# Optimization experiments

Measured on AMD Instinct MI355X. Metric: run time of the kernel, lower is better.

Reference implementation:

```python
import jax, jax.numpy as jnp
import numpy as np

B = 1024          # global batch
D = 512           # embedding_size
C = 100000        # num_classes (sum over 8 shards)
S = 64.0          # ArcFace scale
M = 0.5           # ArcFace additive angular margin
EPS = 1e-30


def setup_inputs() -> dict:
    key = jax.random.key(0)
    k1, k2, k3 = jax.random.split(key, 3)
    embeddings = jax.random.normal(k1, (B, D), dtype=jnp.float32)
    weight = jax.random.normal(k2, (C, D), dtype=jnp.float32)
    labels = jax.random.randint(k3, (B,), 0, C, dtype=jnp.int64)
    return {"embeddings": embeddings, "weight": weight, "labels": labels}


def reference(embeddings, weight, labels):
    # normalize(embeddings), normalize(weight) -> cosine logits
    ne = embeddings * jax.lax.rsqrt(jnp.sum(embeddings * embeddings, axis=1, keepdims=True))
    nw = weight * jax.lax.rsqrt(jnp.sum(weight * weight, axis=1, keepdims=True))
    logits = jnp.clip(jnp.einsum("bd,cd->bc", ne, nw), -1.0, 1.0)  # [B, C]

    rows = jnp.arange(B)
    target_logit = logits[rows, labels]
    # ArcFace: cos(theta + m), theta+m clipped to pi (insightface CombinedMarginLoss m2)
    theta = jnp.arccos(jnp.clip(target_logit, -1.0, 1.0))
    new_target = jnp.cos(jnp.minimum(theta + M, jnp.float32(np.pi)))
    logits = logits.at[rows, labels].set(new_target) * S

    # FusedDistCrossEntropy (single-device equivalent): stable softmax,
    # gather target prob, loss = -mean(log(clamp(p_target, 1e-30)))
    logp = jax.nn.log_softmax(logits, axis=1)
    p_target = jnp.exp(logp[rows, labels])
    loss = -jnp.mean(jnp.log(jnp.maximum(p_target, EPS)))
    return loss
```

## Files before the change

kernel.cpp:

```cpp
#include <hip/hip_runtime.h>
#include <hip/hip_bf16.h>
#include <math.h>
#include <stdint.h>

#define B_BATCH   1024
#define D_DIM     512
#define C_CLASSES 100000
#define BM        128
#define BN        128
#define BK        32
#define KITERS    (D_DIM / BK)
#define MTILES    (B_BATCH / BM)
#define NTILES    ((C_CLASSES + BN - 1) / BN)
#define NGROUPS   98
#define GRID_G    (8 * 8 * NGROUPS)
#define WBLK      (C_CLASSES / 8)
#define ABLK      (B_BATCH / 8)
#define LOG2E     1.44269504088896340736f
#define COSM      0.87758256189037276f
#define SINM      0.47942553860420301f
#define NEG_LOG_EPS 69.07755278982137f

typedef short bf16x8 __attribute__((ext_vector_type(8)));
typedef float f32x4  __attribute__((ext_vector_type(4)));

static __device__ __forceinline__ unsigned short f2bf(float f) {
    unsigned int u = __builtin_bit_cast(unsigned int, f);
    u += 0x7fffu + ((u >> 16) & 1u);
    return (unsigned short)(u >> 16);
}

static __device__ __forceinline__ unsigned int pk_rne(float lo, float hi) {
    return (unsigned int)f2bf(lo) | ((unsigned int)f2bf(hi) << 16);
}

static __device__ __forceinline__ unsigned int pk_bf16_trunc(float lo, float hi) {
    return __builtin_amdgcn_perm(__builtin_bit_cast(unsigned int, hi),
                                 __builtin_bit_cast(unsigned int, lo),
                                 0x07060302u);
}

static __device__ __forceinline__ void gld16(const unsigned short* g, unsigned short* l) {
    __builtin_amdgcn_global_load_lds(
        (const __attribute__((address_space(1))) unsigned int*)g,
        (__attribute__((address_space(3))) unsigned int*)l, 16, 0, 0);
}

__global__ __launch_bounds__(256) void prep(const float* __restrict__ W,
                                            const float* __restrict__ E,
                                            unsigned short* __restrict__ Wbf,
                                            unsigned short* __restrict__ Abf,
                                            float* __restrict__ out) {
    const int blk  = blockIdx.x;
    const int wave = threadIdx.x >> 6;
    const int lane = threadIdx.x & 63;
    const bool isW = blk < WBLK;
    if (!isW && blk == WBLK && threadIdx.x == 0) *out = 0.f;

    const float* src = isW ? W : E;
    unsigned short* dst = isW ? Wbf : Abf;
    const int r0 = (isW ? blk : blk - WBLK) * 8 + wave * 2;
    const int r1 = r0 + 1;

    const float4* s0 = (const float4*)(src + (size_t)r0 * D_DIM);
    const float4* s1 = (const float4*)(src + (size_t)r1 * D_DIM);
    float4 a0 = s0[2 * lane], a1 = s0[2 * lane + 1];
    float4 b0 = s1[2 * lane], b1 = s1[2 * lane + 1];

    float sa = a0.x*a0.x + a0.y*a0.y + a0.z*a0.z + a0.w*a0.w
             + a1.x*a1.x + a1.y*a1.y + a1.z*a1.z + a1.w*a1.w;
    float sb = b0.x*b0.x + b0.y*b0.y + b0.z*b0.z + b0.w*b0.w
             + b1.x*b1.x + b1.y*b1.y + b1.z*b1.z + b1.w*b1.w;
    #pragma unroll
    for (int off = 1; off < 64; off <<= 1) {
        sa += __shfl_xor(sa, off);
        sb += __shfl_xor(sb, off);
    }
    float ia = rsqrtf(sa), ib = rsqrtf(sb);
    a0.x *= ia; a0.y *= ia; a0.z *= ia; a0.w *= ia;
    a1.x *= ia; a1.y *= ia; a1.z *= ia; a1.w *= ia;
    b0.x *= ib; b0.y *= ib; b0.z *= ib; b0.w *= ib;
    b1.x *= ib; b1.y *= ib; b1.z *= ib; b1.w *= ib;

    uint4 oa, ob;
    if (isW) {
        oa = (uint4){pk_bf16_trunc(a0.x, a0.y), pk_bf16_trunc(a0.z, a0.w),
                     pk_bf16_trunc(a1.x, a1.y), pk_bf16_trunc(a1.z, a1.w)};
        ob = (uint4){pk_bf16_trunc(b0.x, b0.y), pk_bf16_trunc(b0.z, b0.w),
                     pk_bf16_trunc(b1.x, b1.y), pk_bf16_trunc(b1.z, b1.w)};
    } else {
        oa = (uint4){pk_rne(a0.x, a0.y), pk_rne(a0.z, a0.w),
                     pk_rne(a1.x, a1.y), pk_rne(a1.z, a1.w)};
        ob = (uint4){pk_rne(b0.x, b0.y), pk_rne(b0.z, b0.w),
                     pk_rne(b1.x, b1.y), pk_rne(b1.z, b1.w)};
    }
    ((uint4*)(dst + (size_t)r0 * D_DIM))[lane] = oa;
    ((uint4*)(dst + (size_t)r1 * D_DIM))[lane] = ob;
}

static __device__ __forceinline__ float epi_term(float accv, int col, int lab,
                                                 float* __restrict__ st, int srow) {
    float c = fminf(1.f, fmaxf(-1.f, accv));
    if (col >= C_CLASSES) return 0.f;
    float s = c * 64.0f;
    if (col == lab) {
        float sn = sqrtf(fmaxf(0.f, 1.f - c * c));
        float nm = c * COSM - sn * SINM;
        if (c < -COSM) nm = -1.f;
        s = nm * 64.0f;
        st[srow] = s;
    }
    return exp2f((s - 64.0f) * LOG2E);
}

__global__ __launch_bounds__(256, 4) void gemm_cos(const unsigned short* __restrict__ Abf,
                                                   const unsigned short* __restrict__ Wbf,
                                                   const int* __restrict__ labels,
                                                   float* __restrict__ st,
                                                   float* __restrict__ partial) {
    __shared__ unsigned short As[BM * BK];
    __shared__ unsigned short Bs[BN * BK];
    __shared__ float rowSum[BM];
    __shared__ int   labs[BM];

    const int id = blockIdx.x;
    const int x  = id & 7;
    const int s  = id >> 3;
    const int mt = s & 7;
    const int y  = x + 8 * (s >> 3);
    if (y >= NTILES) return;
    const int m0 = mt * BM;
    const int n0 = y * BN;

    const int tid = threadIdx.x;
    if (tid < BM) { labs[tid] = labels[m0 + tid]; rowSum[tid] = 0.f; }

    const int lane = tid & 63;
    const int wave = tid >> 6;
    const int wm = wave & 1, wn = wave >> 1;
    const int l15 = lane & 15, quad = lane >> 4;

    const int rsub = lane >> 2;
    const int cg   = (lane & 3) * 8;
    const int c0 = wave * 2, c1 = wave * 2 + 1;
    const unsigned short* gA0 = Abf + (size_t)(m0 + c0 * 16 + rsub) * D_DIM + cg;
    const unsigned short* gA1 = Abf + (size_t)(m0 + c1 * 16 + rsub) * D_DIM + cg;
    const int bR0 = min(n0 + c0 * 16 + rsub, C_CLASSES - 1);
    const int bR1 = min(n0 + c1 * 16 + rsub, C_CLASSES - 1);
    const unsigned short* gB0 = Wbf + (size_t)bR0 * D_DIM + cg;
    const unsigned short* gB1 = Wbf + (size_t)bR1 * D_DIM + cg;
    unsigned short* lA0 = &As[c0 * 512];
    unsigned short* lA1 = &As[c1 * 512];
    unsigned short* lB0 = &Bs[c0 * 512];
    unsigned short* lB1 = &Bs[c1 * 512];

    const f32x4 z = (f32x4){0.f, 0.f, 0.f, 0.f};
    f32x4 a00 = z, a01 = z, a02 = z, a03 = z;
    f32x4 a10 = z, a11 = z, a12 = z, a13 = z;
    f32x4 a20 = z, a21 = z, a22 = z, a23 = z;
    f32x4 a30 = z, a31 = z, a32 = z, a33 = z;

    const int aro = (wm * 64 + l15) * BK + quad * 8;
    const int bro = (wn * 64 + l15) * BK + quad * 8;

    for (int kk = 0; kk < KITERS; ++kk) {
        __syncthreads();
        gld16(gA0, lA0); gld16(gA1, lA1);
        gld16(gB0, lB0); gld16(gB1, lB1);
        gA0 += BK; gA1 += BK; gB0 += BK; gB1 += BK;
        __syncthreads();

        bf16x8 af0 = *(const bf16x8*)&As[aro];
        bf16x8 af1 = *(const bf16x8*)&As[aro + 16 * BK];
        bf16x8 af2 = *(const bf16x8*)&As[aro + 32 * BK];
        bf16x8 af3 = *(const bf16x8*)&As[aro + 48 * BK];
        bf16x8 bf0 = *(const bf16x8*)&Bs[bro];
        bf16x8 bf1 = *(const bf16x8*)&Bs[bro + 16 * BK];
        bf16x8 bf2 = *(const bf16x8*)&Bs[bro + 32 * BK];
        bf16x8 bf3 = *(const bf16x8*)&Bs[bro + 48 * BK];

        a00 = __builtin_amdgcn_mfma_f32_16x16x32_bf16(af0, bf0, a00, 0, 0, 0);
        a01 = __builtin_amdgcn_mfma_f32_16x16x32_bf16(af0, bf1, a01, 0, 0, 0);
        a02 = __builtin_amdgcn_mfma_f32_16x16x32_bf16(af0, bf2, a02, 0, 0, 0);
        a03 = __builtin_amdgcn_mfma_f32_16x16x32_bf16(af0, bf3, a03, 0, 0, 0);
        a10 = __builtin_amdgcn_mfma_f32_16x16x32_bf16(af1, bf0, a10, 0, 0, 0);
        a11 = __builtin_amdgcn_mfma_f32_16x16x32_bf16(af1, bf1, a11, 0, 0, 0);
        a12 = __builtin_amdgcn_mfma_f32_16x16x32_bf16(af1, bf2, a12, 0, 0, 0);
        a13 = __builtin_amdgcn_mfma_f32_16x16x32_bf16(af1, bf3, a13, 0, 0, 0);
        a20 = __builtin_amdgcn_mfma_f32_16x16x32_bf16(af2, bf0, a20, 0, 0, 0);
        a21 = __builtin_amdgcn_mfma_f32_16x16x32_bf16(af2, bf1, a21, 0, 0, 0);
        a22 = __builtin_amdgcn_mfma_f32_16x16x32_bf16(af2, bf2, a22, 0, 0, 0);
        a23 = __builtin_amdgcn_mfma_f32_16x16x32_bf16(af2, bf3, a23, 0, 0, 0);
        a30 = __builtin_amdgcn_mfma_f32_16x16x32_bf16(af3, bf0, a30, 0, 0, 0);
        a31 = __builtin_amdgcn_mfma_f32_16x16x32_bf16(af3, bf1, a31, 0, 0, 0);
        a32 = __builtin_amdgcn_mfma_f32_16x16x32_bf16(af3, bf2, a32, 0, 0, 0);
        a33 = __builtin_amdgcn_mfma_f32_16x16x32_bf16(af3, bf3, a33, 0, 0, 0);
    }

    const int colbase = n0 + wn * 64 + l15;

    #define EPIROW(A0, A1, A2, A3, MI)                                         \
    {                                                                          \
        _Pragma("unroll")                                                      \
        for (int r = 0; r < 4; ++r) {                                          \
            const int rloc = wm * 64 + (MI) * 16 + quad * 4 + r;               \
            const int lab = labs[rloc];                                        \
            float part = 0.f;                                                  \
            part += epi_term((A0)[r], colbase,      lab, st, m0 + rloc);       \
            part += epi_term((A1)[r], colbase + 16, lab, st, m0 + rloc);       \
            part += epi_term((A2)[r], colbase + 32, lab, st, m0 + rloc);       \
            part += epi_term((A3)[r], colbase + 48, lab, st, m0 + rloc);       \
            part += __shfl_xor(part, 1);                                       \
            part += __shfl_xor(part, 2);                                       \
            part += __shfl_xor(part, 4);                                       \
            part += __shfl_xor(part, 8);                                       \
            if (l15 == 0) atomicAdd(&rowSum[rloc], part);                      \
        }                                                                      \
    }

    EPIROW(a00, a01, a02, a03, 0)
    EPIROW(a10, a11, a12, a13, 1)
    EPIROW(a20, a21, a22, a23, 2)
    EPIROW(a30, a31, a32, a33, 3)
    #undef EPIROW

    __syncthreads();
    if (tid < BM) partial[(size_t)(m0 + tid) * NTILES + y] = rowSum[tid];
}

__global__ __launch_bounds__(64) void reduce_loss(const float* __restrict__ partial,
                                                  const float* __restrict__ st,
                                                  float* __restrict__ out) {
    const int b = blockIdx.x;
    const int l = threadIdx.x;
    const float* row = partial + (size_t)b * NTILES;
    float L = 0.f;
    for (int t = l; t < NTILES; t += 64) L += row[t];
    #pragma unroll
    for (int off = 1; off < 64; off <<= 1) L += __shfl_xor(L, off);
    if (l == 0) {
        float logp = st[b] - 64.0f - logf(L);
        float lossb = fminf(-logp, NEG_LOG_EPS) * (1.0f / (float)B_BATCH);
        atomicAdd(out, lossb);
    }
}

extern "C" void kernel_launch(void* const* d_in, const int* in_sizes, int n_in,
                              void* d_out, int out_size, void* d_ws, size_t ws_size,
                              hipStream_t stream) {
    const float* emb = (const float*)d_in[0];
    const float* wgt = (const float*)d_in[1];
    const int*   lab = (const int*)d_in[2];
    float* out = (float*)d_out;
    char* ws = (char*)d_ws;

    const size_t WBF_B = (size_t)C_CLASSES * D_DIM * 2;
    const size_t ABF_B = (size_t)B_BATCH * D_DIM * 2;

    unsigned short* Wbf = (unsigned short*)ws;
    unsigned short* Abf = (unsigned short*)(ws + WBF_B);
    float* st      = (float*)(ws + WBF_B + ABF_B);
    float* partial = (float*)(ws + WBF_B + ABF_B + 4096);

    prep<<<WBLK + ABLK, 256, 0, stream>>>(wgt, emb, Wbf, Abf, out);
    gemm_cos<<<GRID_G, 256, 0, stream>>>(Abf, Wbf, lab, st, partial);
    reduce_loss<<<B_BATCH, 64, 0, stream>>>(partial, st, out);
}
```

Before: 452.4 us.

## Double GEMM K-tile to 64 and add XOR-swizzled LDS layout

Raises the per-iteration K slice from 32 to 64, which halves the number of barrier pairs in the main loop and gives two MFMA groups per synchronisation. The global-to-LDS staging is rebuilt with an XOR swizzle on 16-byte column chunks so that the 128-byte LDS rows can be read by the MFMA fragments without bank conflicts. LDS footprint per block doubles, which may reduce occupancy, and the loop is still single-buffered, so loads are not overlapped with compute.

```diff
diff --git a/kernel.cpp b/kernel.cpp
--- a/kernel.cpp
+++ b/kernel.cpp
@@ -8,7 +8,7 @@
 #define C_CLASSES 100000
 #define BM        128
 #define BN        128
-#define BK        32
+#define BK        64
 #define KITERS    (D_DIM / BK)
 #define MTILES    (B_BATCH / BM)
 #define NTILES    ((C_CLASSES + BN - 1) / BN)
@@ -140,19 +140,22 @@
     const int wm = wave & 1, wn = wave >> 1;
     const int l15 = lane & 15, quad = lane >> 4;
 
-    const int rsub = lane >> 2;
-    const int cg   = (lane & 3) * 8;
-    const int c0 = wave * 2, c1 = wave * 2 + 1;
-    const unsigned short* gA0 = Abf + (size_t)(m0 + c0 * 16 + rsub) * D_DIM + cg;
-    const unsigned short* gA1 = Abf + (size_t)(m0 + c1 * 16 + rsub) * D_DIM + cg;
-    const int bR0 = min(n0 + c0 * 16 + rsub, C_CLASSES - 1);
-    const int bR1 = min(n0 + c1 * 16 + rsub, C_CLASSES - 1);
-    const unsigned short* gB0 = Wbf + (size_t)bR0 * D_DIM + cg;
-    const unsigned short* gB1 = Wbf + (size_t)bR1 * D_DIM + cg;
-    unsigned short* lA0 = &As[c0 * 512];
-    unsigned short* lA1 = &As[c1 * 512];
-    unsigned short* lB0 = &Bs[c0 * 512];
-    unsigned short* lB1 = &Bs[c1 * 512];
+    const int rIn = lane >> 3;
+    const int csl = (((lane & 7) ^ rIn) << 4);
+    const char* gA[4];
+    const char* gB[4];
+    unsigned short* lA[4];
+    unsigned short* lB[4];
+    #pragma unroll
+    for (int c = 0; c < 4; ++c) {
+        const int chunk = wave * 4 + c;
+        const int row = chunk * 8 + rIn;
+        gA[c] = (const char*)Abf + (size_t)(m0 + row) * (D_DIM * 2) + csl;
+        const int bRow = min(n0 + row, C_CLASSES - 1);
+        gB[c] = (const char*)Wbf + (size_t)bRow * (D_DIM * 2) + csl;
+        lA[c] = &As[chunk * 512];
+        lB[c] = &Bs[chunk * 512];
+    }
 
     const f32x4 z = (f32x4){0.f, 0.f, 0.f, 0.f};
     f32x4 a00 = z, a01 = z, a02 = z, a03 = z;
@@ -160,41 +163,48 @@
     f32x4 a20 = z, a21 = z, a22 = z, a23 = z;
     f32x4 a30 = z, a31 = z, a32 = z, a33 = z;
 
-    const int aro = (wm * 64 + l15) * BK + quad * 8;
-    const int bro = (wn * 64 + l15) * BK + quad * 8;
+    const char* baseA = (const char*)As + (size_t)(wm * 64 + l15) * 128;
+    const char* baseB = (const char*)Bs + (size_t)(wn * 64 + l15) * 128;
+    const int q0 = ((quad ^ (l15 & 7)) << 4);
 
     for (int kk = 0; kk < KITERS; ++kk) {
         __syncthreads();
-        gld16(gA0, lA0); gld16(gA1, lA1);
-        gld16(gB0, lB0); gld16(gB1, lB1);
-        gA0 += BK; gA1 += BK; gB0 += BK; gB1 += BK;
+        #pragma unroll
+        for (int c = 0; c < 4; ++c) {
+            gld16((const unsigned short*)gA[c], lA[c]); gA[c] += 2 * BK;
+            gld16((const unsigned short*)gB[c], lB[c]); gB[c] += 2 * BK;
+        }
         __syncthreads();
 
-        bf16x8 af0 = *(const bf16x8*)&As[aro];
-        bf16x8 af1 = *(const bf16x8*)&As[aro + 16 * BK];
-        bf16x8 af2 = *(const bf16x8*)&As[aro + 32 * BK];
-        bf16x8 af3 = *(const bf16x8*)&As[aro + 48 * BK];
-        bf16x8 bf0 = *(const bf16x8*)&Bs[bro];
-        bf16x8 bf1 = *(const bf16x8*)&Bs[bro + 16 * BK];
-        bf16x8 bf2 = *(const bf16x8*)&Bs[bro + 32 * BK];
-        bf16x8 bf3 = *(const bf16x8*)&Bs[bro + 48 * BK];
-
-        a00 = __builtin_amdgcn_mfma_f32_16x16x32_bf16(af0, bf0, a00, 0, 0, 0);
-        a01 = __builtin_amdgcn_mfma_f32_16x16x32_bf16(af0, bf1, a01, 0, 0, 0);
-        a02 = __builtin_amdgcn_mfma_f32_16x16x32_bf16(af0, bf2, a02, 0, 0, 0);
-        a03 = __builtin_amdgcn_mfma_f32_16x16x32_bf16(af0, bf3, a03, 0, 0, 0);
-        a10 = __builtin_amdgcn_mfma_f32_16x16x32_bf16(af1, bf0, a10, 0, 0, 0);
-        a11 = __builtin_amdgcn_mfma_f32_16x16x32_bf16(af1, bf1, a11, 0, 0, 0);
-        a12 = __builtin_amdgcn_mfma_f32_16x16x32_bf16(af1, bf2, a12, 0, 0, 0);
-        a13 = __builtin_amdgcn_mfma_f32_16x16x32_bf16(af1, bf3, a13, 0, 0, 0);
-        a20 = __builtin_amdgcn_mfma_f32_16x16x32_bf16(af2, bf0, a20, 0, 0, 0);
-        a21 = __builtin_amdgcn_mfma_f32_16x16x32_bf16(af2, bf1, a21, 0, 0, 0);
-        a22 = __builtin_amdgcn_mfma_f32_16x16x32_bf16(af2, bf2, a22, 0, 0, 0);
-        a23 = __builtin_amdgcn_mfma_f32_16x16x32_bf16(af2, bf3, a23, 0, 0, 0);
-        a30 = __builtin_amdgcn_mfma_f32_16x16x32_bf16(af3, bf0, a30, 0, 0, 0);
-        a31 = __builtin_amdgcn_mfma_f32_16x16x32_bf16(af3, bf1, a31, 0, 0, 0);
-        a32 = __builtin_amdgcn_mfma_f32_16x16x32_bf16(af3, bf2, a32, 0, 0, 0);
-        a33 = __builtin_amdgcn_mfma_f32_16x16x32_bf16(af3, bf3, a33, 0, 0, 0);
+        #pragma unroll
+        for (int kh = 0; kh < 2; ++kh) {
+            const int off = q0 ^ (kh << 6);
+            bf16x8 af0 = *(const bf16x8*)(baseA          + off);
+            bf16x8 af1 = *(const bf16x8*)(baseA + 2048   + off);
+            bf16x8 af2 = *(const bf16x8*)(baseA + 4096   + off);
+            bf16x8 af3 = *(const bf16x8*)(baseA + 6144   + off);
+            bf16x8 bf0 = *(const bf16x8*)(baseB          + off);
+            bf16x8 bf1 = *(const bf16x8*)(baseB + 2048   + off);
+            bf16x8 bf2 = *(const bf16x8*)(baseB + 4096   + off);
+            bf16x8 bf3 = *(const bf16x8*)(baseB + 6144   + off);
+
+            a00 = __builtin_amdgcn_mfma_f32_16x16x32_bf16(af0, bf0, a00, 0, 0, 0);
+            a01 = __builtin_amdgcn_mfma_f32_16x16x32_bf16(af0, bf1, a01, 0, 0, 0);
+            a02 = __builtin_amdgcn_mfma_f32_16x16x32_bf16(af0, bf2, a02, 0, 0, 0);
+            a03 = __builtin_amdgcn_mfma_f32_16x16x32_bf16(af0, bf3, a03, 0, 0, 0);
+            a10 = __builtin_amdgcn_mfma_f32_16x16x32_bf16(af1, bf0, a10, 0, 0, 0);
+            a11 = __builtin_amdgcn_mfma_f32_16x16x32_bf16(af1, bf1, a11, 0, 0, 0);
+            a12 = __builtin_amdgcn_mfma_f32_16x16x32_bf16(af1, bf2, a12, 0, 0, 0);
+            a13 = __builtin_amdgcn_mfma_f32_16x16x32_bf16(af1, bf3, a13, 0, 0, 0);
+            a20 = __builtin_amdgcn_mfma_f32_16x16x32_bf16(af2, bf0, a20, 0, 0, 0);
+            a21 = __builtin_amdgcn_mfma_f32_16x16x32_bf16(af2, bf1, a21, 0, 0, 0);
+            a22 = __builtin_amdgcn_mfma_f32_16x16x32_bf16(af2, bf2, a22, 0, 0, 0);
+            a23 = __builtin_amdgcn_mfma_f32_16x16x32_bf16(af2, bf3, a23, 0, 0, 0);
+            a30 = __builtin_amdgcn_mfma_f32_16x16x32_bf16(af3, bf0, a30, 0, 0, 0);
+            a31 = __builtin_amdgcn_mfma_f32_16x16x32_bf16(af3, bf1, a31, 0, 0, 0);
+            a32 = __builtin_amdgcn_mfma_f32_16x16x32_bf16(af3, bf2, a32, 0, 0, 0);
+            a33 = __builtin_amdgcn_mfma_f32_16x16x32_bf16(af3, bf3, a33, 0, 0, 0);
+        }
     }
 
     const int colbase = n0 + wn * 64 + l15;
```

Result: no change. 459.1 us (+1.5%).
